# Performance work log

Hardware: AMD Instinct MI355X
Metric: run time of the kernel (lower is better)

## Reference

```python
import jax, jax.numpy as jnp
import numpy as np

N, M, E, H = 4096, 16384, 512, 8
D = E // H  # head dim = 64


def _rms(x, g, eps=1e-6):
    return x * jax.lax.rsqrt(jnp.mean(jnp.square(x), axis=-1, keepdims=True) + eps) * g


def _split(x):
    # (rows, E) -> (rows, H, D)
    return x.reshape(x.shape[0], H, D)


def _sdpa(q, k, v):
    # Faithful to the source layout: SDPA on (rows, H, D) tensors, i.e. per-row
    # attention over the H heads (tiny HxH softmax per node).
    s = jnp.einsum('nhd,ngd->nhg', q, k) / jnp.sqrt(jnp.asarray(D, q.dtype))
    a = jax.nn.softmax(s, axis=-1)
    return jnp.einsum('nhg,ngd->nhd', a, v).reshape(-1, E)


def setup_inputs() -> dict:
    key = jax.random.key(0)
    ks = jax.random.split(key, 25)
    w = lambda k, s, sc: jax.random.normal(k, s, dtype=jnp.float32) * sc
    se = 1.0 / np.sqrt(E)   # Linear(E, E) init scale
    sm = 1.0 / np.sqrt(M)   # Linear(M, N) init scale
    inp = {
        'x_node': jax.random.normal(ks[0], (N, E), dtype=jnp.float32),
        'x_edge': jax.random.normal(ks[1], (M, E), dtype=jnp.float32),
        # sparse-ish binary adjacency, avg degree ~8
        'adj': (jax.random.uniform(ks[2], (N, N)) < 0.002).astype(jnp.float32),
        # per-branch QKV weights (4 separate MultiHeadAttention modules)
        'Wq_hh': w(ks[3], (E, E), se), 'Wk_hh': w(ks[4], (E, E), se), 'Wv_hh': w(ks[5], (E, E), se),
        'Wq_ee': w(ks[6], (E, E), se), 'Wk_ee': w(ks[7], (E, E), se), 'Wv_ee': w(ks[8], (E, E), se),
        'Wq_he': w(ks[9], (E, E), se), 'Wk_he': w(ks[10], (E, E), se), 'Wv_he': w(ks[11], (E, E), se),
        'Wq_eh': w(ks[12], (E, E), se), 'Wk_eh': w(ks[13], (E, E), se), 'Wv_eh': w(ks[14], (E, E), se),
        # shape_proj (edges -> nodes) weights, one per module that uses it
        'Wp1_he': w(ks[15], (N, M), sm),
        'Wp1_eh': w(ks[16], (N, M), sm),
        'Wp1_ee': w(ks[17], (N, M), sm),
        # RMSNorm gains
        'g_n': jnp.ones((E,), jnp.float32),
        'g_e': jnp.ones((E,), jnp.float32),
        'g2': jnp.ones((E,), jnp.float32),
        # FeedForward
        'Wf1': w(ks[18], (E, 4 * E), se), 'bf1': jnp.zeros((4 * E,), jnp.float32),
        'Wf2': w(ks[19], (4 * E, E), 1.0 / np.sqrt(4 * E)), 'bf2': jnp.zeros((E,), jnp.float32),
    }
    return inp


def reference(x_node, x_edge, adj,
              Wq_hh, Wk_hh, Wv_hh, Wq_ee, Wk_ee, Wv_ee,
              Wq_he, Wk_he, Wv_he, Wq_eh, Wk_eh, Wv_eh,
              Wp1_he, Wp1_eh, Wp1_ee,
              g_n, g_e, g2, Wf1, bf1, Wf2, bf2):
    h = _rms(x_node, g_n)   # (N, E)
    e = _rms(x_edge, g_e)   # (M, E)

    # hh: adjacency injected into the node query branch
    q = jnp.einsum('nm,mhd->nhd', adj, _split(h @ Wq_hh))
    out_hh = _sdpa(q, _split(h @ Wk_hh), _split(h @ Wv_hh))

    # ee: edge queries/keys projected to node rows via shape_proj
    q = jnp.einsum('nm,mhd->nhd', Wp1_ee, _split(e @ Wq_ee))
    k = jnp.einsum('nm,mhd->nhd', Wp1_ee, _split(e @ Wk_ee))
    out_ee = _sdpa(q, k, _split(h @ Wv_ee))

    # eh: edge query projected to node rows, node key
    q = jnp.einsum('nm,mhd->nhd', Wp1_eh, _split(e @ Wq_eh))
    out_eh = _sdpa(q, _split(h @ Wk_eh), _split(h @ Wv_eh))

    # he: node query, edge key projected to node rows
    k = jnp.einsum('nm,mhd->nhd', Wp1_he, _split(e @ Wk_he))
    out_he = _sdpa(_split(h @ Wq_he), k, _split(h @ Wv_he))

    x = out_hh + out_ee + out_eh + out_he          # (N, E)
    y = _rms(x, g2)
    return jax.nn.gelu(y @ Wf1 + bf1, approximate=False) @ Wf2 + bf2
```

## Files before the change

kernel.cpp:

```cpp
#include <hip/hip_runtime.h>
#include <cstdint>


typedef unsigned short u16;
typedef __bf16 bf16x8 __attribute__((ext_vector_type(8)));
typedef float f32x4 __attribute__((ext_vector_type(4)));

__device__ __forceinline__ u16 f2bf(float f) {
    unsigned u = __float_as_uint(f);
    return (u16)((u + 0x7fffu + ((u >> 16) & 1u)) >> 16);
}
__device__ __forceinline__ float bf2f(u16 u) { return __uint_as_float(((unsigned)u) << 16); }
__device__ __forceinline__ float gelu_exact(float x) {
    return 0.5f * x * (1.0f + erff(x * 0.70710678118654752f));
}

__device__ __forceinline__ void gload_lds16(const u16* g, u16* l) {
    __builtin_amdgcn_global_load_lds(
        (const __attribute__((address_space(1))) unsigned int*)(uintptr_t)g,
        (__attribute__((address_space(3))) unsigned int*)(unsigned int)(uintptr_t)l,
        16, 0, 0);
}

__device__ __forceinline__ void swz_block(int& bx, int& by, int& bz) {
    const int nx = gridDim.x, ny = gridDim.y;
    const int nwg = nx * ny * gridDim.z;
    int lin = blockIdx.x + nx * (blockIdx.y + ny * blockIdx.z);
    const int chunk = nwg >> 3;
    lin = (lin & 7) * chunk + (lin >> 3);
    bx = lin % nx;
    lin /= nx;
    by = lin % ny;
    bz = lin / ny;
}

template <bool SWZ>
__global__ __launch_bounds__(256) void cvt_f32_bf16(const float* __restrict__ in,
                                                    u16* __restrict__ out, size_t n8) {
    size_t i = (size_t)blockIdx.x * 256 + threadIdx.x;
    size_t stride = (size_t)gridDim.x * 256;
    for (; i < n8; i += stride) {
        float4 a = ((const float4*)in)[i * 2];
        float4 b = ((const float4*)in)[i * 2 + 1];
        u16 r[8] = {f2bf(a.x), f2bf(a.y), f2bf(a.z), f2bf(a.w),
                    f2bf(b.x), f2bf(b.y), f2bf(b.z), f2bf(b.w)};
        size_t o = i;
        if constexpr (SWZ) o = (i & ~(size_t)63) | ((i & 63) ^ ((i >> 6) & 3));
        ((uint4*)out)[o] = *(const uint4*)r;
    }
}

__global__ __launch_bounds__(256) void transpose_cvt(const float* __restrict__ in,
                                                     u16* __restrict__ out, int R, int C) {
    __shared__ float tile[32][33];
    int c0 = blockIdx.x * 32, r0 = blockIdx.y * 32;
    int tx = threadIdx.x & 31, ty = threadIdx.x >> 5;
#pragma unroll
    for (int i = 0; i < 4; ++i)
        tile[ty + i * 8][tx] = in[(size_t)(r0 + ty + i * 8) * C + c0 + tx];
    __syncthreads();
#pragma unroll
    for (int i = 0; i < 4; ++i) {
        int orow = c0 + ty + i * 8;
        out[(size_t)orow * R + ((r0 + tx) ^ ((orow & 3) << 3))] = f2bf(tile[tx][ty + i * 8]);
    }
}

struct W12 { const float* in[12]; u16* out[12]; };
__global__ __launch_bounds__(256) void transpose_cvt12(W12 w) {
    __shared__ float tile[32][33];
    const float* in = w.in[blockIdx.z];
    u16* out = w.out[blockIdx.z];
    int c0 = blockIdx.x * 32, r0 = blockIdx.y * 32;
    int tx = threadIdx.x & 31, ty = threadIdx.x >> 5;
#pragma unroll
    for (int i = 0; i < 4; ++i)
        tile[ty + i * 8][tx] = in[(size_t)(r0 + ty + i * 8) * 512 + c0 + tx];
    __syncthreads();
#pragma unroll
    for (int i = 0; i < 4; ++i) {
        int orow = c0 + ty + i * 8;
        out[(size_t)orow * 512 + ((r0 + tx) ^ ((orow & 3) << 3))] = f2bf(tile[tx][ty + i * 8]);
    }
}

__global__ __launch_bounds__(256) void transpose_u16(const u16* __restrict__ in,
                                                     u16* __restrict__ out, int R, int C) {
    __shared__ u16 tile[32][34];
    int c0 = blockIdx.x * 32, r0 = blockIdx.y * 32;
    int tx = threadIdx.x & 31, ty = threadIdx.x >> 5;
#pragma unroll
    for (int i = 0; i < 4; ++i)
        tile[ty + i * 8][tx] = in[(size_t)(r0 + ty + i * 8) * C + c0 + tx];
    __syncthreads();
#pragma unroll
    for (int i = 0; i < 4; ++i) {
        int orow = c0 + ty + i * 8;
        out[(size_t)orow * R + ((r0 + tx) ^ ((orow & 3) << 3))] = tile[tx][ty + i * 8];
    }
}

template <bool SWZ>
__global__ __launch_bounds__(256) void rmsnorm_bf16(const float* __restrict__ x,
                                                    const float* __restrict__ g,
                                                    u16* __restrict__ out) {
    int row = blockIdx.x, tid = threadIdx.x;
    const float* xr = x + (size_t)row * 512;
    float2 v = *(const float2*)(xr + tid * 2);
    float ss = v.x * v.x + v.y * v.y;
#pragma unroll
    for (int o = 32; o; o >>= 1) ss += __shfl_down(ss, o);
    __shared__ float red[4];
    if ((tid & 63) == 0) red[tid >> 6] = ss;
    __syncthreads();
    float tot = red[0] + red[1] + red[2] + red[3];
    float rs = rsqrtf(tot * (1.0f / 512.0f) + 1e-6f);
    unsigned pack = (unsigned)f2bf(v.x * rs * g[tid * 2]) |
                    ((unsigned)f2bf(v.y * rs * g[tid * 2 + 1]) << 16);
    int o32 = SWZ ? (tid ^ ((row & 3) << 2)) : tid;
    ((unsigned*)out)[(size_t)row * 256 + o32] = pack;
}

__global__ __launch_bounds__(256) void adj_spmm(const float* __restrict__ adj,
                                                const u16* __restrict__ h,
                                                u16* __restrict__ out) {
    const int wave = threadIdx.x >> 6, lane = threadIdx.x & 63;
    const int n = blockIdx.x * 4 + wave;
    const float* arow = adj + (size_t)n * 4096;
    float acc[8] = {0.f, 0.f, 0.f, 0.f, 0.f, 0.f, 0.f, 0.f};
    for (int j = 0; j < 64; ++j) {
        float v = arow[j * 64 + lane];
        unsigned long long mask = __ballot(v != 0.0f);
        while (mask) {
            int bit = __ffsll((long long)mask) - 1;
            mask &= mask - 1;
            int m = j * 64 + bit;
            float w = __shfl(v, bit);
            int cs = (lane & ~3) | ((lane & 3) ^ (m & 3));
            uint4 q = *(const uint4*)(h + (size_t)m * 512 + cs * 8);
            const u16* qu = (const u16*)&q;
#pragma unroll
            for (int t = 0; t < 8; ++t) acc[t] += w * bf2f(qu[t]);
        }
    }
    int co = (lane & ~3) | ((lane & 3) ^ (n & 3));
    u16 r[8];
#pragma unroll
    for (int t = 0; t < 8; ++t) r[t] = f2bf(acc[t]);
    *(uint4*)(out + (size_t)n * 512 + co * 8) = *(const uint4*)r;
}

template <int MODE>
__device__ __forceinline__ void gemm_tile_body(const u16* __restrict__ A,
                                               const u16* __restrict__ Bt,
                                               int N, int K, int k_begin, int k_end,
                                               int rowStart, int colStart,
                                               void* __restrict__ C,
                                               const float* __restrict__ bias) {
    __shared__ u16 Asm[128 * 32];
    __shared__ u16 Bsm[128 * 32];
    const int tid = threadIdx.x;
    const int wave = tid >> 6, lane = tid & 63;
    const int wr = wave >> 1, wc = wave & 1;

    f32x4 acc[4][4];
#pragma unroll
    for (int m = 0; m < 4; ++m)
#pragma unroll
        for (int n = 0; n < 4; ++n) acc[m][n] = f32x4{0.f, 0.f, 0.f, 0.f};

    const int off0 = (wave * 2 + 0) * 1024 + lane * 16;
    const int off1 = (wave * 2 + 1) * 1024 + lane * 16;
    const int r0 = off0 >> 6, k0e = (off0 & 63) >> 1;
    const int r1 = off1 >> 6, k1e = (off1 & 63) >> 1;
    const size_t Arow0 = (size_t)(rowStart + r0) * K + k0e;
    const size_t Arow1 = (size_t)(rowStart + r1) * K + k1e;
    const size_t Brow0 = (size_t)(colStart + r0) * K + k0e;
    const size_t Brow1 = (size_t)(colStart + r1) * K + k1e;
    u16* As0 = &Asm[(wave * 2 + 0) * 512];
    u16* As1 = &Asm[(wave * 2 + 1) * 512];
    u16* Bs0 = &Bsm[(wave * 2 + 0) * 512];
    u16* Bs1 = &Bsm[(wave * 2 + 1) * 512];

    const int rsel = lane & 15, ksel = lane >> 4;
    const int fsw = ((ksel ^ (rsel & 3)) << 3);

    for (int kk = k_begin; kk < k_end; kk += 32) {
        gload_lds16(A + Arow0 + kk, As0);
        gload_lds16(A + Arow1 + kk, As1);
        gload_lds16(Bt + Brow0 + kk, Bs0);
        gload_lds16(Bt + Brow1 + kk, Bs1);
        __syncthreads();
        bf16x8 aF[4], bF[4];
#pragma unroll
        for (int m = 0; m < 4; ++m)
            aF[m] = *(const bf16x8*)&Asm[(wr * 64 + m * 16 + rsel) * 32 + fsw];
#pragma unroll
        for (int n = 0; n < 4; ++n)
            bF[n] = *(const bf16x8*)&Bsm[(wc * 64 + n * 16 + rsel) * 32 + fsw];
#pragma unroll
        for (int m = 0; m < 4; ++m)
#pragma unroll
            for (int n = 0; n < 4; ++n)
                acc[m][n] = __builtin_amdgcn_mfma_f32_16x16x32_bf16(aF[m], bF[n], acc[m][n], 0, 0, 0);
        __syncthreads();
    }

    const int cq = (lane >> 4) * 4, cr = lane & 15;
#pragma unroll
    for (int m = 0; m < 4; ++m) {
#pragma unroll
        for (int n = 0; n < 4; ++n) {
            int col = colStart + wc * 64 + n * 16 + cr;
#pragma unroll
            for (int j = 0; j < 4; ++j) {
                int row = rowStart + wr * 64 + m * 16 + cq + j;
                float v = acc[m][n][j];
                if constexpr (MODE == 0) {
                    ((u16*)C)[(size_t)row * N + col] = f2bf(v);
                } else if constexpr (MODE == 1) {
                    v = gelu_exact(v + bias[col]);
                    ((u16*)C)[(size_t)row * N + (col ^ ((row & 3) << 3))] = f2bf(v);
                } else {
                    if (bias) v += bias[col];
                    atomicAdd(&((float*)C)[(size_t)row * N + col], v);
                }
            }
        }
    }
}

template <int MODE>
__global__ __launch_bounds__(256, 2) void gemm_bt(const u16* __restrict__ A,
                                                  const u16* __restrict__ Bt,
                                                  void* __restrict__ C,
                                                  const float* __restrict__ bias,
                                                  int N, int K, int kLen) {
    int bx, by, bz;
    swz_block(bx, by, bz);
    const float* bb = (MODE == 3) ? ((bz == 0) ? bias : nullptr) : bias;
    int kb = bz * kLen;
    gemm_tile_body<MODE>(A, Bt, N, K, kb, kb + kLen, by * 128, bx * 128, C, bb);
}

struct Small12 { const u16* A[12]; const u16* W[12]; u16* C[12]; };
__global__ __launch_bounds__(256, 2) void gemm_small12(Small12 s) {
    int bx, by, bz;
    swz_block(bx, by, bz);
    gemm_tile_body<0>(s.A[bz], s.W[bz], 512, 512, 0, 512, by * 128, bx * 128, s.C[bz], nullptr);
}

struct Big3 { const float* A[3]; };
__global__ __launch_bounds__(256, 2) void gemm_f32a(Big3 ba, const u16* __restrict__ Bt,
                                                    float* __restrict__ C0, int K,
                                                    int zPerMat, int kLen) {
    __shared__ u16 Asm[128 * 32];
    __shared__ u16 Bsm[128 * 32];
    int bx, by, bz;
    swz_block(bx, by, bz);
    const int m = bz / zPerMat, ks = bz - m * zPerMat;
    const float* __restrict__ A = ba.A[m];
    float* __restrict__ C = C0 + (size_t)m * (4096 * 512);
    const int rowStart = by * 128, colStart = bx * 128;
    const int k0 = ks * kLen, kEnd = k0 + kLen;

    const int tid = threadIdx.x;
    const int wave = tid >> 6, lane = tid & 63;
    const int wr = wave >> 1, wc = wave & 1;

    f32x4 acc[4][4];
#pragma unroll
    for (int mm = 0; mm < 4; ++mm)
#pragma unroll
        for (int n = 0; n < 4; ++n) acc[mm][n] = f32x4{0.f, 0.f, 0.f, 0.f};

    const int r = tid >> 1, half = tid & 1;
    const float4* Ap4 = (const float4*)(A + (size_t)(rowStart + r) * K + half * 16);
    const int sw = (r & 7) << 4;
    u16* aw0 = (u16*)((char*)Asm + (((r * 64 + half * 32) ^ sw)));
    u16* aw1 = (u16*)((char*)Asm + (((r * 64 + half * 32 + 16) ^ sw)));

    const int off0 = (wave * 2 + 0) * 1024 + lane * 16;
    const int off1 = (wave * 2 + 1) * 1024 + lane * 16;
    const int br0 = off0 >> 6, bk0 = (off0 & 63) >> 1;
    const int br1 = off1 >> 6, bk1 = (off1 & 63) >> 1;
    const u16* Bp0 = Bt + (size_t)(colStart + br0) * K + bk0;
    const u16* Bp1 = Bt + (size_t)(colStart + br1) * K + bk1;
    u16* Bs0 = &Bsm[(wave * 2 + 0) * 512];
    u16* Bs1 = &Bsm[(wave * 2 + 1) * 512];

    const int rsel = lane & 15, ksel = lane >> 4;
    const int fsw = ((ksel ^ (rsel & 3)) << 3);

    float4 a0, a1, a2, a3;
    {
        const float4* p = Ap4 + (k0 >> 2);
        a0 = p[0]; a1 = p[1]; a2 = p[2]; a3 = p[3];
    }
    for (int kk = k0; kk < kEnd; kk += 32) {
        gload_lds16(Bp0 + kk, Bs0);
        gload_lds16(Bp1 + kk, Bs1);
        bf16x8 c0, c1;
        c0[0] = (__bf16)a0.x; c0[1] = (__bf16)a0.y; c0[2] = (__bf16)a0.z; c0[3] = (__bf16)a0.w;
        c0[4] = (__bf16)a1.x; c0[5] = (__bf16)a1.y; c0[6] = (__bf16)a1.z; c0[7] = (__bf16)a1.w;
        c1[0] = (__bf16)a2.x; c1[1] = (__bf16)a2.y; c1[2] = (__bf16)a2.z; c1[3] = (__bf16)a2.w;
        c1[4] = (__bf16)a3.x; c1[5] = (__bf16)a3.y; c1[6] = (__bf16)a3.z; c1[7] = (__bf16)a3.w;
        *(bf16x8*)aw0 = c0;
        *(bf16x8*)aw1 = c1;
        if (kk + 32 < kEnd) {
            const float4* p = Ap4 + ((kk + 32) >> 2);
            a0 = p[0]; a1 = p[1]; a2 = p[2]; a3 = p[3];
        }
        __syncthreads();
        bf16x8 aF[4], bF[4];
#pragma unroll
        for (int mm = 0; mm < 4; ++mm) {
            int R = wr * 64 + mm * 16 + rsel;
            aF[mm] = *(const bf16x8*)((char*)Asm + ((R * 64 + ksel * 16) ^ ((R & 7) << 4)));
        }
#pragma unroll
        for (int n = 0; n < 4; ++n)
            bF[n] = *(const bf16x8*)&Bsm[(wc * 64 + n * 16 + rsel) * 32 + fsw];
#pragma unroll
        for (int mm = 0; mm < 4; ++mm)
#pragma unroll
            for (int n = 0; n < 4; ++n)
                acc[mm][n] = __builtin_amdgcn_mfma_f32_16x16x32_bf16(aF[mm], bF[n], acc[mm][n], 0, 0, 0);
        __syncthreads();
    }

    const int cq = (lane >> 4) * 4, cr = lane & 15;
#pragma unroll
    for (int mm = 0; mm < 4; ++mm)
#pragma unroll
        for (int n = 0; n < 4; ++n) {
            int col = colStart + wc * 64 + n * 16 + cr;
#pragma unroll
            for (int j = 0; j < 4; ++j) {
                int row = rowStart + wr * 64 + mm * 16 + cq + j;
                atomicAdd(&C[(size_t)row * 512 + col], acc[mm][n][j]);
            }
        }
}

struct SP12 { const u16* p[12]; };
__global__ __launch_bounds__(256) void sdpa_fused(SP12 sp, const float* __restrict__ g2,
                                                  u16* __restrict__ y) {
    __shared__ float qb[4][8][65], kb[4][8][65], vb[4][8][65];
    __shared__ float aw[4][64];
    __shared__ float red[4];
    const int n = blockIdx.x, tid = threadIdx.x;
    const size_t base = (size_t)n * 512;
    const int e0 = tid * 2, hs = e0 >> 6, ds = e0 & 63;

#pragma unroll
    for (int br = 0; br < 4; ++br) {
        unsigned u;
        u = *(const unsigned*)(sp.p[br * 3 + 0] + base + e0);
        qb[br][hs][ds] = bf2f(u & 0xffffu); qb[br][hs][ds + 1] = bf2f(u >> 16);
        u = *(const unsigned*)(sp.p[br * 3 + 1] + base + e0);
        kb[br][hs][ds] = bf2f(u & 0xffffu); kb[br][hs][ds + 1] = bf2f(u >> 16);
        u = *(const unsigned*)(sp.p[br * 3 + 2] + base + e0);
        vb[br][hs][ds] = bf2f(u & 0xffffu); vb[br][hs][ds + 1] = bf2f(u >> 16);
    }
    __syncthreads();

    const int b = tid >> 6, h = (tid >> 3) & 7, g = tid & 7;
    float s = 0.f;
    const float* qr = &qb[b][h][0];
    const float* kr = &kb[b][g][0];
#pragma unroll
    for (int j = 0; j < 64; ++j) s += qr[j] * kr[j];
    s *= 0.125f;
    float mx = s;
#pragma unroll
    for (int o = 1; o < 8; o <<= 1) mx = fmaxf(mx, __shfl_xor(mx, o));
    float p = expf(s - mx);
    float sm = p;
#pragma unroll
    for (int o = 1; o < 8; o <<= 1) sm += __shfl_xor(sm, o);
    aw[b][(h << 3) | g] = p / sm;
    __syncthreads();

    float o0 = 0.f, o1 = 0.f;
#pragma unroll
    for (int bb = 0; bb < 4; ++bb)
#pragma unroll
        for (int gg = 0; gg < 8; ++gg) {
            float a = aw[bb][(hs << 3) | gg];
            o0 += a * vb[bb][gg][ds];
            o1 += a * vb[bb][gg][ds + 1];
        }

    float ss = o0 * o0 + o1 * o1;
#pragma unroll
    for (int o = 32; o; o >>= 1) ss += __shfl_down(ss, o);
    if ((tid & 63) == 0) red[tid >> 6] = ss;
    __syncthreads();
    float tot = red[0] + red[1] + red[2] + red[3];
    float rs = rsqrtf(tot * (1.0f / 512.0f) + 1e-6f);
    unsigned pack = (unsigned)f2bf(o0 * rs * g2[e0]) | ((unsigned)f2bf(o1 * rs * g2[e0 + 1]) << 16);
    ((unsigned*)y)[(size_t)n * 256 + (tid ^ ((n & 3) << 2))] = pack;
}

extern "C" void kernel_launch(void* const* d_in, const int* in_sizes, int n_in,
                              void* d_out, int out_size, void* d_ws, size_t ws_size,
                              hipStream_t stream) {
    (void)in_sizes; (void)n_in; (void)out_size; (void)ws_size;
    const int N = 4096, M = 16384, E = 512;

    const float* x_node = (const float*)d_in[0];
    const float* x_edge = (const float*)d_in[1];
    const float* adj    = (const float*)d_in[2];
    const float* Wp1_he = (const float*)d_in[15];
    const float* Wp1_eh = (const float*)d_in[16];
    const float* Wp1_ee = (const float*)d_in[17];
    const float* g_n = (const float*)d_in[18];
    const float* g_e = (const float*)d_in[19];
    const float* g2  = (const float*)d_in[20];
    const float* Wf1 = (const float*)d_in[21];
    const float* bf1 = (const float*)d_in[22];
    const float* Wf2 = (const float*)d_in[23];
    const float* bf2 = (const float*)d_in[24];

    char* p = (char*)d_ws;
    auto alloc = [&](size_t b) { char* r = p; p += (b + 255) & ~(size_t)255; return r; };
    const size_t NP = (size_t)N * E;
    const size_t WSZ = (size_t)E * E;
    u16* h    = (u16*)alloc(NP * 2);
    u16* e    = (u16*)alloc((size_t)M * E * 2);
    u16* eT   = (u16*)alloc((size_t)M * E * 2);
    u16* Wt   = (u16*)alloc(12 * WSZ * 2);
    u16* Wf1T = (u16*)alloc((size_t)2048 * 512 * 2);
    u16* Wf2T = (u16*)alloc((size_t)512 * 2048 * 2);
    float* F3 = (float*)alloc(3 * NP * 4);
    u16* P3b  = (u16*)alloc(3 * NP * 2);
    u16* Ahb  = (u16*)alloc(NP * 2);
    u16* S12  = (u16*)alloc(12 * NP * 2);
    u16* y    = (u16*)alloc(NP * 2);
    u16* t    = (u16*)alloc((size_t)N * 2048 * 2);

    W12 w12;
    for (int i = 0; i < 12; ++i) { w12.in[i] = (const float*)d_in[3 + i]; w12.out[i] = Wt + i * WSZ; }
    transpose_cvt12<<<dim3(16, 16, 12), 256, 0, stream>>>(w12);
    transpose_cvt<<<dim3(64, 16), 256, 0, stream>>>(Wf1, Wf1T, 512, 2048);
    transpose_cvt<<<dim3(16, 64), 256, 0, stream>>>(Wf2, Wf2T, 2048, 512);

    rmsnorm_bf16<true><<<N, 256, 0, stream>>>(x_node, g_n, h);
    rmsnorm_bf16<false><<<M, 256, 0, stream>>>(x_edge, g_e, e);
    transpose_u16<<<dim3(16, 512), 256, 0, stream>>>(e, eT, M, 512);
    adj_spmm<<<1024, 256, 0, stream>>>(adj, h, Ahb);

    hipMemsetAsync(F3, 0, 3 * NP * 4, stream);
    Big3 bp; bp.A[0] = Wp1_ee; bp.A[1] = Wp1_eh; bp.A[2] = Wp1_he;
    gemm_f32a<<<dim3(4, 32, 12), 256, 0, stream>>>(bp, eT, F3, M, 4, 4096);
    cvt_f32_bf16<true><<<2048, 256, 0, stream>>>(F3, P3b, 3 * NP / 8);
    const u16* Peeb = P3b + 0 * NP;
    const u16* Pehb = P3b + 1 * NP;
    const u16* Pheb = P3b + 2 * NP;

    Small12 sb;
    const u16* aList[12] = {Ahb, h, h, Peeb, Peeb, h, Pehb, h, h, h, Pheb, h};
    const int wList[12]  = {0, 1, 2, 3, 4, 5, 9, 10, 11, 6, 7, 8};
    for (int i = 0; i < 12; ++i) {
        sb.A[i] = aList[i];
        sb.W[i] = Wt + wList[i] * WSZ;
        sb.C[i] = S12 + i * NP;
    }
    gemm_small12<<<dim3(4, 32, 12), 256, 0, stream>>>(sb);

    SP12 sp;
    for (int i = 0; i < 12; ++i) sp.p[i] = S12 + i * NP;
    sdpa_fused<<<N, 256, 0, stream>>>(sp, g2, y);

    gemm_bt<1><<<dim3(16, 32, 1), 256, 0, stream>>>(y, Wf1T, t, bf1, 2048, 512, 512);
    hipMemsetAsync(d_out, 0, NP * 4, stream);
    gemm_bt<3><<<dim3(4, 32, 2), 256, 0, stream>>>(t, Wf2T, d_out, bf2, 512, 2048, 1024);
}
```

Baseline: 638.5 us.

## Double-buffer GEMM LDS tiles with vmcnt-based barriers and retune swizzle

```diff
diff --git a/kernel.cpp b/kernel.cpp
--- a/kernel.cpp
+++ b/kernel.cpp
@@ -21,6 +21,8 @@
         (__attribute__((address_space(3))) unsigned int*)(unsigned int)(uintptr_t)l,
         16, 0, 0);
 }
+
+#define WAITBAR(N) asm volatile("s_waitcnt vmcnt(" #N ") lgkmcnt(0)\ns_barrier" ::: "memory")
 
 __device__ __forceinline__ void swz_block(int& bx, int& by, int& bz) {
     const int nx = gridDim.x, ny = gridDim.y;
@@ -45,7 +47,7 @@
         u16 r[8] = {f2bf(a.x), f2bf(a.y), f2bf(a.z), f2bf(a.w),
                     f2bf(b.x), f2bf(b.y), f2bf(b.z), f2bf(b.w)};
         size_t o = i;
-        if constexpr (SWZ) o = (i & ~(size_t)63) | ((i & 63) ^ ((i >> 6) & 3));
+        if constexpr (SWZ) o = (i & ~(size_t)63) | ((i & 63) ^ ((i >> 7) & 3));
         ((uint4*)out)[o] = *(const uint4*)r;
     }
 }
@@ -62,7 +64,7 @@
 #pragma unroll
     for (int i = 0; i < 4; ++i) {
         int orow = c0 + ty + i * 8;
-        out[(size_t)orow * R + ((r0 + tx) ^ ((orow & 3) << 3))] = f2bf(tile[tx][ty + i * 8]);
+        out[(size_t)orow * R + ((r0 + tx) ^ (((orow >> 1) & 3) << 3))] = f2bf(tile[tx][ty + i * 8]);
     }
 }
 
@@ -80,7 +82,7 @@
 #pragma unroll
     for (int i = 0; i < 4; ++i) {
         int orow = c0 + ty + i * 8;
-        out[(size_t)orow * 512 + ((r0 + tx) ^ ((orow & 3) << 3))] = f2bf(tile[tx][ty + i * 8]);
+        out[(size_t)orow * 512 + ((r0 + tx) ^ (((orow >> 1) & 3) << 3))] = f2bf(tile[tx][ty + i * 8]);
     }
 }
 
@@ -96,7 +98,7 @@
 #pragma unroll
     for (int i = 0; i < 4; ++i) {
         int orow = c0 + ty + i * 8;
-        out[(size_t)orow * R + ((r0 + tx) ^ ((orow & 3) << 3))] = tile[tx][ty + i * 8];
+        out[(size_t)orow * R + ((r0 + tx) ^ (((orow >> 1) & 3) << 3))] = tile[tx][ty + i * 8];
     }
 }
 
@@ -117,7 +119,7 @@
     float rs = rsqrtf(tot * (1.0f / 512.0f) + 1e-6f);
     unsigned pack = (unsigned)f2bf(v.x * rs * g[tid * 2]) |
                     ((unsigned)f2bf(v.y * rs * g[tid * 2 + 1]) << 16);
-    int o32 = SWZ ? (tid ^ ((row & 3) << 2)) : tid;
+    int o32 = SWZ ? (tid ^ (((row >> 1) & 3) << 2)) : tid;
     ((unsigned*)out)[(size_t)row * 256 + o32] = pack;
 }
 
@@ -136,14 +138,14 @@
             mask &= mask - 1;
             int m = j * 64 + bit;
             float w = __shfl(v, bit);
-            int cs = (lane & ~3) | ((lane & 3) ^ (m & 3));
+            int cs = (lane & ~3) | ((lane & 3) ^ ((m >> 1) & 3));
             uint4 q = *(const uint4*)(h + (size_t)m * 512 + cs * 8);
             const u16* qu = (const u16*)&q;
 #pragma unroll
             for (int t = 0; t < 8; ++t) acc[t] += w * bf2f(qu[t]);
         }
     }
-    int co = (lane & ~3) | ((lane & 3) ^ (n & 3));
+    int co = (lane & ~3) | ((lane & 3) ^ ((n >> 1) & 3));
     u16 r[8];
 #pragma unroll
     for (int t = 0; t < 8; ++t) r[t] = f2bf(acc[t]);
@@ -157,8 +159,8 @@
                                                int rowStart, int colStart,
                                                void* __restrict__ C,
                                                const float* __restrict__ bias) {
-    __shared__ u16 Asm[128 * 32];
-    __shared__ u16 Bsm[128 * 32];
+    __shared__ u16 Asm[2 * 4096];
+    __shared__ u16 Bsm[2 * 4096];
     const int tid = threadIdx.x;
     const int wave = tid >> 6, lane = tid & 63;
     const int wr = wave >> 1, wc = wave & 1;
@@ -177,34 +179,48 @@
     const size_t Arow1 = (size_t)(rowStart + r1) * K + k1e;
     const size_t Brow0 = (size_t)(colStart + r0) * K + k0e;
     const size_t Brow1 = (size_t)(colStart + r1) * K + k1e;
-    u16* As0 = &Asm[(wave * 2 + 0) * 512];
-    u16* As1 = &Asm[(wave * 2 + 1) * 512];
-    u16* Bs0 = &Bsm[(wave * 2 + 0) * 512];
-    u16* Bs1 = &Bsm[(wave * 2 + 1) * 512];
+    const int ws0 = (wave * 2 + 0) * 512, ws1 = (wave * 2 + 1) * 512;
 
     const int rsel = lane & 15, ksel = lane >> 4;
-    const int fsw = ((ksel ^ (rsel & 3)) << 3);
-
-    for (int kk = k_begin; kk < k_end; kk += 32) {
-        gload_lds16(A + Arow0 + kk, As0);
-        gload_lds16(A + Arow1 + kk, As1);
-        gload_lds16(Bt + Brow0 + kk, Bs0);
-        gload_lds16(Bt + Brow1 + kk, Bs1);
-        __syncthreads();
+    const int fsw = (ksel ^ ((rsel >> 1) & 3)) << 3;
+
+    auto STAGE = [&](int buf, int kk) {
+        u16* as = Asm + buf * 4096;
+        u16* bs = Bsm + buf * 4096;
+        gload_lds16(A + Arow0 + kk, as + ws0);
+        gload_lds16(A + Arow1 + kk, as + ws1);
+        gload_lds16(Bt + Brow0 + kk, bs + ws0);
+        gload_lds16(Bt + Brow1 + kk, bs + ws1);
+    };
+    auto COMPUTE = [&](int buf) {
+        const u16* as = Asm + buf * 4096;
+        const u16* bs = Bsm + buf * 4096;
         bf16x8 aF[4], bF[4];
 #pragma unroll
         for (int m = 0; m < 4; ++m)
-            aF[m] = *(const bf16x8*)&Asm[(wr * 64 + m * 16 + rsel) * 32 + fsw];
+            aF[m] = *(const bf16x8*)&as[(wr * 64 + m * 16 + rsel) * 32 + fsw];
 #pragma unroll
         for (int n = 0; n < 4; ++n)
-            bF[n] = *(const bf16x8*)&Bsm[(wc * 64 + n * 16 + rsel) * 32 + fsw];
+            bF[n] = *(const bf16x8*)&bs[(wc * 64 + n * 16 + rsel) * 32 + fsw];
 #pragma unroll
         for (int m = 0; m < 4; ++m)
 #pragma unroll
             for (int n = 0; n < 4; ++n)
                 acc[m][n] = __builtin_amdgcn_mfma_f32_16x16x32_bf16(aF[m], bF[n], acc[m][n], 0, 0, 0);
-        __syncthreads();
-    }
+    };
+
+    const int nt = (k_end - k_begin) >> 5;
+    STAGE(0, k_begin);
+    int cur = 0;
+    for (int t = 0; t < nt - 1; ++t) {
+        STAGE(cur ^ 1, k_begin + (t + 1) * 32);
+        WAITBAR(4);
+        COMPUTE(cur);
+        WAITBAR(63);
+        cur ^= 1;
+    }
+    WAITBAR(0);
+    COMPUTE(cur);
 
     const int cq = (lane >> 4) * 4, cr = lane & 15;
 #pragma unroll
@@ -220,7 +236,7 @@
                     ((u16*)C)[(size_t)row * N + col] = f2bf(v);
                 } else if constexpr (MODE == 1) {
                     v = gelu_exact(v + bias[col]);
-                    ((u16*)C)[(size_t)row * N + (col ^ ((row & 3) << 3))] = f2bf(v);
+                    ((u16*)C)[(size_t)row * N + (col ^ (((row >> 1) & 3) << 3))] = f2bf(v);
                 } else {
                     if (bias) v += bias[col];
                     atomicAdd(&((float*)C)[(size_t)row * N + col], v);
@@ -231,11 +247,11 @@
 }
 
 template <int MODE>
-__global__ __launch_bounds__(256, 2) void gemm_bt(const u16* __restrict__ A,
-                                                  const u16* __restrict__ Bt,
-                                                  void* __restrict__ C,
-                                                  const float* __restrict__ bias,
-                                                  int N, int K, int kLen) {
+__global__ __launch_bounds__(256) void gemm_bt(const u16* __restrict__ A,
+                                               const u16* __restrict__ Bt,
+                                               void* __restrict__ C,
+                                               const float* __restrict__ bias,
+                                               int N, int K, int kLen) {
     int bx, by, bz;
     swz_block(bx, by, bz);
     const float* bb = (MODE == 3) ? ((bz == 0) ? bias : nullptr) : bias;
@@ -244,25 +260,26 @@
 }
 
 struct Small12 { const u16* A[12]; const u16* W[12]; u16* C[12]; };
-__global__ __launch_bounds__(256, 2) void gemm_small12(Small12 s) {
+__global__ __launch_bounds__(256) void gemm_small12(Small12 s) {
     int bx, by, bz;
     swz_block(bx, by, bz);
     gemm_tile_body<0>(s.A[bz], s.W[bz], 512, 512, 0, 512, by * 128, bx * 128, s.C[bz], nullptr);
 }
 
 struct Big3 { const float* A[3]; };
-__global__ __launch_bounds__(256, 2) void gemm_f32a(Big3 ba, const u16* __restrict__ Bt,
-                                                    float* __restrict__ C0, int K,
-                                                    int zPerMat, int kLen) {
-    __shared__ u16 Asm[128 * 32];
-    __shared__ u16 Bsm[128 * 32];
+__global__ __launch_bounds__(256) void gemm_f32a(Big3 ba, const u16* __restrict__ Bt,
+                                                 float* __restrict__ C0, int K,
+                                                 int zPerMat, int kLen) {
+    __shared__ u16 Asm[2 * 4096];
+    __shared__ u16 Bsm[2 * 4096];
     int bx, by, bz;
     swz_block(bx, by, bz);
-    const int m = bz / zPerMat, ks = bz - m * zPerMat;
-    const float* __restrict__ A = ba.A[m];
-    float* __restrict__ C = C0 + (size_t)m * (4096 * 512);
+    const int mat = bz / zPerMat, ks = bz - mat * zPerMat;
+    const float* __restrict__ A = ba.A[mat];
+    float* __restrict__ C = C0 + (size_t)mat * (4096 * 512);
     const int rowStart = by * 128, colStart = bx * 128;
     const int k0 = ks * kLen, kEnd = k0 + kLen;
+    const int nt = kLen >> 5;
 
     const int tid = threadIdx.x;
     const int wave = tid >> 6, lane = tid & 63;
@@ -277,8 +294,8 @@
     const int r = tid >> 1, half = tid & 1;
     const float4* Ap4 = (const float4*)(A + (size_t)(rowStart + r) * K + half * 16);
     const int sw = (r & 7) << 4;
-    u16* aw0 = (u16*)((char*)Asm + (((r * 64 + half * 32) ^ sw)));
-    u16* aw1 = (u16*)((char*)Asm + (((r * 64 + half * 32 + 16) ^ sw)));
+    const int awo0 = (r * 64 + half * 32) ^ sw;
+    const int awo1 = (r * 64 + half * 32 + 16) ^ sw;
 
     const int off0 = (wave * 2 + 0) * 1024 + lane * 16;
     const int off1 = (wave * 2 + 1) * 1024 + lane * 16;
@@ -286,48 +303,74 @@
     const int br1 = off1 >> 6, bk1 = (off1 & 63) >> 1;
     const u16* Bp0 = Bt + (size_t)(colStart + br0) * K + bk0;
     const u16* Bp1 = Bt + (size_t)(colStart + br1) * K + bk1;
-    u16* Bs0 = &Bsm[(wave * 2 + 0) * 512];
-    u16* Bs1 = &Bsm[(wave * 2 + 1) * 512];
+    const int ws0 = (wave * 2 + 0) * 512, ws1 = (wave * 2 + 1) * 512;
 
     const int rsel = lane & 15, ksel = lane >> 4;
-    const int fsw = ((ksel ^ (rsel & 3)) << 3);
-
-    float4 a0, a1, a2, a3;
-    {
-        const float4* p = Ap4 + (k0 >> 2);
-        a0 = p[0]; a1 = p[1]; a2 = p[2]; a3 = p[3];
-    }
-    for (int kk = k0; kk < kEnd; kk += 32) {
-        gload_lds16(Bp0 + kk, Bs0);
-        gload_lds16(Bp1 + kk, Bs1);
+    const int fsw = (ksel ^ ((rsel >> 1) & 3)) << 3;
+
+    float4 eA0, eA1, eA2, eA3;
+    float4 oA0, oA1, oA2, oA3;
+
+    auto WRITE_A = [&](int buf, float4 a0, float4 a1, float4 a2, float4 a3) {
         bf16x8 c0, c1;
         c0[0] = (__bf16)a0.x; c0[1] = (__bf16)a0.y; c0[2] = (__bf16)a0.z; c0[3] = (__bf16)a0.w;
         c0[4] = (__bf16)a1.x; c0[5] = (__bf16)a1.y; c0[6] = (__bf16)a1.z; c0[7] = (__bf16)a1.w;
         c1[0] = (__bf16)a2.x; c1[1] = (__bf16)a2.y; c1[2] = (__bf16)a2.z; c1[3] = (__bf16)a2.w;
         c1[4] = (__bf16)a3.x; c1[5] = (__bf16)a3.y; c1[6] = (__bf16)a3.z; c1[7] = (__bf16)a3.w;
-        *(bf16x8*)aw0 = c0;
-        *(bf16x8*)aw1 = c1;
-        if (kk + 32 < kEnd) {
-            const float4* p = Ap4 + ((kk + 32) >> 2);
-            a0 = p[0]; a1 = p[1]; a2 = p[2]; a3 = p[3];
-        }
-        __syncthreads();
+        char* base = (char*)(Asm + buf * 4096);
+        *(bf16x8*)(base + awo0) = c0;
+        *(bf16x8*)(base + awo1) = c1;
+    };
+    auto COMPUTE = [&](int buf) {
+        const u16* as = Asm + buf * 4096;
+        const u16* bs = Bsm + buf * 4096;
         bf16x8 aF[4], bF[4];
 #pragma unroll
         for (int mm = 0; mm < 4; ++mm) {
             int R = wr * 64 + mm * 16 + rsel;
-            aF[mm] = *(const bf16x8*)((char*)Asm + ((R * 64 + ksel * 16) ^ ((R & 7) << 4)));
+            aF[mm] = *(const bf16x8*)((const char*)as + ((R * 64 + ksel * 16) ^ ((R & 7) << 4)));
         }
 #pragma unroll
         for (int n = 0; n < 4; ++n)
-            bF[n] = *(const bf16x8*)&Bsm[(wc * 64 + n * 16 + rsel) * 32 + fsw];
+            bF[n] = *(const bf16x8*)&bs[(wc * 64 + n * 16 + rsel) * 32 + fsw];
 #pragma unroll
         for (int mm = 0; mm < 4; ++mm)
 #pragma unroll
             for (int n = 0; n < 4; ++n)
                 acc[mm][n] = __builtin_amdgcn_mfma_f32_16x16x32_bf16(aF[mm], bF[n], acc[mm][n], 0, 0, 0);
-        __syncthreads();
-    }
+    };
+
+    {
+        const float4* p = Ap4 + (k0 >> 2);
+        eA0 = p[0]; eA1 = p[1]; eA2 = p[2]; eA3 = p[3];
+        gload_lds16(Bp0 + k0, Bsm + ws0);
+        gload_lds16(Bp1 + k0, Bsm + ws1);
+        int kk1 = k0 + 32;
+        if (kk1 > kEnd - 32) kk1 = kEnd - 32;
+        const float4* q = Ap4 + (kk1 >> 2);
+        oA0 = q[0]; oA1 = q[1]; oA2 = q[2]; oA3 = q[3];
+        WRITE_A(0, eA0, eA1, eA2, eA3);
+    }
+
+    int cur = 0;
+    for (int t = 0; t < nt - 1; ++t) {
+        int kk2 = k0 + (t + 2) * 32;
+        if (kk2 > kEnd - 32) kk2 = kEnd - 32;
+        const float4* p = Ap4 + (kk2 >> 2);
+        if (t & 1) { oA0 = p[0]; oA1 = p[1]; oA2 = p[2]; oA3 = p[3]; }
+        else       { eA0 = p[0]; eA1 = p[1]; eA2 = p[2]; eA3 = p[3]; }
+        int kk1 = k0 + (t + 1) * 32;
+        gload_lds16(Bp0 + kk1, Bsm + (cur ^ 1) * 4096 + ws0);
+        gload_lds16(Bp1 + kk1, Bsm + (cur ^ 1) * 4096 + ws1);
+        if (t & 1) WRITE_A(cur ^ 1, eA0, eA1, eA2, eA3);
+        else       WRITE_A(cur ^ 1, oA0, oA1, oA2, oA3);
+        WAITBAR(6);
+        COMPUTE(cur);
+        WAITBAR(63);
+        cur ^= 1;
+    }
+    WAITBAR(0);
+    COMPUTE(cur);
 
     const int cq = (lane >> 4) * 4, cr = lane & 15;
 #pragma unroll
@@ -400,7 +443,7 @@
     float tot = red[0] + red[1] + red[2] + red[3];
     float rs = rsqrtf(tot * (1.0f / 512.0f) + 1e-6f);
     unsigned pack = (unsigned)f2bf(o0 * rs * g2[e0]) | ((unsigned)f2bf(o1 * rs * g2[e0 + 1]) << 16);
-    ((unsigned*)y)[(size_t)n * 256 + (tid ^ ((n & 3) << 2))] = pack;
+    ((unsigned*)y)[(size_t)n * 256 + (tid ^ (((n >> 1) & 3) << 2))] = pack;
 }
 
 extern "C" void kernel_launch(void* const* d_in, const int* in_sizes, int n_in,
```

Measured after the change: 807.8 us. 26.5% more time.

## Stream fp32 A tiles into LDS via direct loads and rework swizzle pattern

Applied to the files above, without the earlier changes.

```diff
diff --git a/kernel.cpp b/kernel.cpp
--- a/kernel.cpp
+++ b/kernel.cpp
@@ -15,7 +15,7 @@
     return 0.5f * x * (1.0f + erff(x * 0.70710678118654752f));
 }
 
-__device__ __forceinline__ void gload_lds16(const u16* g, u16* l) {
+__device__ __forceinline__ void gload_lds16(const void* g, void* l) {
     __builtin_amdgcn_global_load_lds(
         (const __attribute__((address_space(1))) unsigned int*)(uintptr_t)g,
         (__attribute__((address_space(3))) unsigned int*)(unsigned int)(uintptr_t)l,
@@ -45,7 +45,7 @@
         u16 r[8] = {f2bf(a.x), f2bf(a.y), f2bf(a.z), f2bf(a.w),
                     f2bf(b.x), f2bf(b.y), f2bf(b.z), f2bf(b.w)};
         size_t o = i;
-        if constexpr (SWZ) o = (i & ~(size_t)63) | ((i & 63) ^ ((i >> 6) & 3));
+        if constexpr (SWZ) o = (i & ~(size_t)63) | ((i & 63) ^ ((i >> 7) & 3));
         ((uint4*)out)[o] = *(const uint4*)r;
     }
 }
@@ -62,7 +62,7 @@
 #pragma unroll
     for (int i = 0; i < 4; ++i) {
         int orow = c0 + ty + i * 8;
-        out[(size_t)orow * R + ((r0 + tx) ^ ((orow & 3) << 3))] = f2bf(tile[tx][ty + i * 8]);
+        out[(size_t)orow * R + ((r0 + tx) ^ (((orow >> 1) & 3) << 3))] = f2bf(tile[tx][ty + i * 8]);
     }
 }
 
@@ -80,7 +80,7 @@
 #pragma unroll
     for (int i = 0; i < 4; ++i) {
         int orow = c0 + ty + i * 8;
-        out[(size_t)orow * 512 + ((r0 + tx) ^ ((orow & 3) << 3))] = f2bf(tile[tx][ty + i * 8]);
+        out[(size_t)orow * 512 + ((r0 + tx) ^ (((orow >> 1) & 3) << 3))] = f2bf(tile[tx][ty + i * 8]);
     }
 }
 
@@ -96,7 +96,7 @@
 #pragma unroll
     for (int i = 0; i < 4; ++i) {
         int orow = c0 + ty + i * 8;
-        out[(size_t)orow * R + ((r0 + tx) ^ ((orow & 3) << 3))] = tile[tx][ty + i * 8];
+        out[(size_t)orow * R + ((r0 + tx) ^ (((orow >> 1) & 3) << 3))] = tile[tx][ty + i * 8];
     }
 }
 
@@ -117,7 +117,7 @@
     float rs = rsqrtf(tot * (1.0f / 512.0f) + 1e-6f);
     unsigned pack = (unsigned)f2bf(v.x * rs * g[tid * 2]) |
                     ((unsigned)f2bf(v.y * rs * g[tid * 2 + 1]) << 16);
-    int o32 = SWZ ? (tid ^ ((row & 3) << 2)) : tid;
+    int o32 = SWZ ? (tid ^ (((row >> 1) & 3) << 2)) : tid;
     ((unsigned*)out)[(size_t)row * 256 + o32] = pack;
 }
 
@@ -136,14 +136,14 @@
             mask &= mask - 1;
             int m = j * 64 + bit;
             float w = __shfl(v, bit);
-            int cs = (lane & ~3) | ((lane & 3) ^ (m & 3));
+            int cs = (lane & ~3) | ((lane & 3) ^ ((m >> 1) & 3));
             uint4 q = *(const uint4*)(h + (size_t)m * 512 + cs * 8);
             const u16* qu = (const u16*)&q;
 #pragma unroll
             for (int t = 0; t < 8; ++t) acc[t] += w * bf2f(qu[t]);
         }
     }
-    int co = (lane & ~3) | ((lane & 3) ^ (n & 3));
+    int co = (lane & ~3) | ((lane & 3) ^ ((n >> 1) & 3));
     u16 r[8];
 #pragma unroll
     for (int t = 0; t < 8; ++t) r[t] = f2bf(acc[t]);
@@ -183,7 +183,7 @@
     u16* Bs1 = &Bsm[(wave * 2 + 1) * 512];
 
     const int rsel = lane & 15, ksel = lane >> 4;
-    const int fsw = ((ksel ^ (rsel & 3)) << 3);
+    const int fsw = (ksel ^ ((rsel >> 1) & 3)) << 3;
 
     for (int kk = k_begin; kk < k_end; kk += 32) {
         gload_lds16(A + Arow0 + kk, As0);
@@ -220,7 +220,7 @@
                     ((u16*)C)[(size_t)row * N + col] = f2bf(v);
                 } else if constexpr (MODE == 1) {
                     v = gelu_exact(v + bias[col]);
-                    ((u16*)C)[(size_t)row * N + (col ^ ((row & 3) << 3))] = f2bf(v);
+                    ((u16*)C)[(size_t)row * N + (col ^ (((row >> 1) & 3) << 3))] = f2bf(v);
                 } else {
                     if (bias) v += bias[col];
                     atomicAdd(&((float*)C)[(size_t)row * N + col], v);
@@ -231,11 +231,11 @@
 }
 
 template <int MODE>
-__global__ __launch_bounds__(256, 2) void gemm_bt(const u16* __restrict__ A,
-                                                  const u16* __restrict__ Bt,
-                                                  void* __restrict__ C,
-                                                  const float* __restrict__ bias,
-                                                  int N, int K, int kLen) {
+__global__ __launch_bounds__(256) void gemm_bt(const u16* __restrict__ A,
+                                               const u16* __restrict__ Bt,
+                                               void* __restrict__ C,
+                                               const float* __restrict__ bias,
+                                               int N, int K, int kLen) {
     int bx, by, bz;
     swz_block(bx, by, bz);
     const float* bb = (MODE == 3) ? ((bz == 0) ? bias : nullptr) : bias;
@@ -244,7 +244,7 @@
 }
 
 struct Small12 { const u16* A[12]; const u16* W[12]; u16* C[12]; };
-__global__ __launch_bounds__(256, 2) void gemm_small12(Small12 s) {
+__global__ __launch_bounds__(256) void gemm_small12(Small12 s) {
     int bx, by, bz;
     swz_block(bx, by, bz);
     gemm_tile_body<0>(s.A[bz], s.W[bz], 512, 512, 0, 512, by * 128, bx * 128, s.C[bz], nullptr);
@@ -254,13 +254,13 @@
 __global__ __launch_bounds__(256, 2) void gemm_f32a(Big3 ba, const u16* __restrict__ Bt,
                                                     float* __restrict__ C0, int K,
                                                     int zPerMat, int kLen) {
-    __shared__ u16 Asm[128 * 32];
+    __shared__ float Afs[128 * 32];
     __shared__ u16 Bsm[128 * 32];
     int bx, by, bz;
     swz_block(bx, by, bz);
-    const int m = bz / zPerMat, ks = bz - m * zPerMat;
-    const float* __restrict__ A = ba.A[m];
-    float* __restrict__ C = C0 + (size_t)m * (4096 * 512);
+    const int mat = bz / zPerMat, ks = bz - mat * zPerMat;
+    const float* __restrict__ A = ba.A[mat];
+    float* __restrict__ C = C0 + (size_t)mat * (4096 * 512);
     const int rowStart = by * 128, colStart = bx * 128;
     const int k0 = ks * kLen, kEnd = k0 + kLen;
 
@@ -274,11 +274,16 @@
 #pragma unroll
         for (int n = 0; n < 4; ++n) acc[mm][n] = f32x4{0.f, 0.f, 0.f, 0.f};
 
-    const int r = tid >> 1, half = tid & 1;
-    const float4* Ap4 = (const float4*)(A + (size_t)(rowStart + r) * K + half * 16);
-    const int sw = (r & 7) << 4;
-    u16* aw0 = (u16*)((char*)Asm + (((r * 64 + half * 32) ^ sw)));
-    u16* aw1 = (u16*)((char*)Asm + (((r * 64 + half * 32 + 16) ^ sw)));
+    const int lrow = lane >> 3;
+    const int slot = (lane & 7) ^ lrow;
+    size_t asrc[4];
+    float* adst[4];
+#pragma unroll
+    for (int i = 0; i < 4; ++i) {
+        int row = wave * 32 + i * 8 + lrow;
+        asrc[i] = (size_t)(rowStart + row) * K + slot * 4;
+        adst[i] = Afs + (wave * 4 + i) * 256 + lane * 4;
+    }
 
     const int off0 = (wave * 2 + 0) * 1024 + lane * 16;
     const int off1 = (wave * 2 + 1) * 1024 + lane * 16;
@@ -290,33 +295,26 @@
     u16* Bs1 = &Bsm[(wave * 2 + 1) * 512];
 
     const int rsel = lane & 15, ksel = lane >> 4;
-    const int fsw = ((ksel ^ (rsel & 3)) << 3);
-
-    float4 a0, a1, a2, a3;
-    {
-        const float4* p = Ap4 + (k0 >> 2);
-        a0 = p[0]; a1 = p[1]; a2 = p[2]; a3 = p[3];
-    }
+    const int fsw = (ksel ^ ((rsel >> 1) & 3)) << 3;
+
     for (int kk = k0; kk < kEnd; kk += 32) {
+#pragma unroll
+        for (int i = 0; i < 4; ++i)
+            gload_lds16(A + asrc[i] + kk, adst[i]);
         gload_lds16(Bp0 + kk, Bs0);
         gload_lds16(Bp1 + kk, Bs1);
-        bf16x8 c0, c1;
-        c0[0] = (__bf16)a0.x; c0[1] = (__bf16)a0.y; c0[2] = (__bf16)a0.z; c0[3] = (__bf16)a0.w;
-        c0[4] = (__bf16)a1.x; c0[5] = (__bf16)a1.y; c0[6] = (__bf16)a1.z; c0[7] = (__bf16)a1.w;
-        c1[0] = (__bf16)a2.x; c1[1] = (__bf16)a2.y; c1[2] = (__bf16)a2.z; c1[3] = (__bf16)a2.w;
-        c1[4] = (__bf16)a3.x; c1[5] = (__bf16)a3.y; c1[6] = (__bf16)a3.z; c1[7] = (__bf16)a3.w;
-        *(bf16x8*)aw0 = c0;
-        *(bf16x8*)aw1 = c1;
-        if (kk + 32 < kEnd) {
-            const float4* p = Ap4 + ((kk + 32) >> 2);
-            a0 = p[0]; a1 = p[1]; a2 = p[2]; a3 = p[3];
-        }
         __syncthreads();
         bf16x8 aF[4], bF[4];
 #pragma unroll
         for (int mm = 0; mm < 4; ++mm) {
             int R = wr * 64 + mm * 16 + rsel;
-            aF[mm] = *(const bf16x8*)((char*)Asm + ((R * 64 + ksel * 16) ^ ((R & 7) << 4)));
+            const char* rb = (const char*)Afs + R * 128;
+            f32x4 lo = *(const f32x4*)(rb + ((((ksel << 1) | 0) ^ (R & 7)) << 4));
+            f32x4 hi = *(const f32x4*)(rb + ((((ksel << 1) | 1) ^ (R & 7)) << 4));
+            aF[mm][0] = (__bf16)lo[0]; aF[mm][1] = (__bf16)lo[1];
+            aF[mm][2] = (__bf16)lo[2]; aF[mm][3] = (__bf16)lo[3];
+            aF[mm][4] = (__bf16)hi[0]; aF[mm][5] = (__bf16)hi[1];
+            aF[mm][6] = (__bf16)hi[2]; aF[mm][7] = (__bf16)hi[3];
         }
 #pragma unroll
         for (int n = 0; n < 4; ++n)
@@ -400,7 +398,7 @@
     float tot = red[0] + red[1] + red[2] + red[3];
     float rs = rsqrtf(tot * (1.0f / 512.0f) + 1e-6f);
     unsigned pack = (unsigned)f2bf(o0 * rs * g2[e0]) | ((unsigned)f2bf(o1 * rs * g2[e0 + 1]) << 16);
-    ((unsigned*)y)[(size_t)n * 256 + (tid ^ ((n & 3) << 2))] = pack;
+    ((unsigned*)y)[(size_t)n * 256 + (tid ^ (((n >> 1) & 3) << 2))] = pack;
 }
 
 extern "C" void kernel_launch(void* const* d_in, const int* in_sizes, int n_in,
```

Result: no change. 638.2 us (-0.0%).
